# Kernel optimization log

Measured on AMD Instinct MI355X. Metric: run time of the kernel, lower is better.

The kernel has to match this reference:

```python
import jax, jax.numpy as jnp
import numpy as np

N = 50000      # atoms
E = 800000     # edges (avg degree 16)
F = 32         # feature channels
NB = 8         # Bessel basis size
RCUT = 20.0    # Angstrom cutoff (covers the 1nm box)
EV2KJ = 96.4853
NM2A = 10.0


def setup_inputs() -> dict:
    key = jax.random.key(0)
    ks = jax.random.split(key, 12)
    return {
        "positions": jax.random.uniform(ks[0], (N, 3), jnp.float32),      # nm
        "masses": jax.random.uniform(ks[1], (N,), jnp.float32),
        "type_embed": jax.random.normal(ks[2], (3, F), jnp.float32),
        "W_rad1": jax.random.normal(ks[3], (NB, F), jnp.float32) * 0.3,
        "b_rad1": jax.random.normal(ks[4], (F,), jnp.float32) * 0.1,
        "W_rad2": jax.random.normal(ks[5], (F, 2 * F), jnp.float32) * 0.3,
        "W_self": jax.random.normal(ks[6], (F, F), jnp.float32) * 0.3,
        "W_out1": jax.random.normal(ks[7], (2 * F, F), jnp.float32) * 0.3,
        "b_out1": jax.random.normal(ks[8], (F,), jnp.float32) * 0.1,
        "W_out2": jax.random.normal(ks[9], (F, 1), jnp.float32) * 0.3,
        "atom_types": jax.random.randint(ks[10], (N,), 0, 3),
        "edge_index": jax.random.randint(ks[11], (2, E), 0, N),
    }


def reference(positions, masses, type_embed, W_rad1, b_rad1, W_rad2,
              W_self, W_out1, b_out1, W_out2, atom_types, edge_index):
    src, dst = edge_index[0], edge_index[1]

    def energy_eV(pos_A):
        rel = pos_A[dst] - pos_A[src]                       # [E,3] gather
        r = jnp.sqrt(jnp.sum(rel * rel, axis=-1) + 1e-12)   # [E]
        rhat = rel / r[:, None]
        # Bessel radial basis with p=6 polynomial cutoff envelope
        x = r / RCUT
        n = jnp.arange(1, NB + 1, dtype=pos_A.dtype)
        basis = jnp.sin(jnp.pi * n[None, :] * x[:, None]) / r[:, None]  # [E,NB]
        p = 6.0
        env = (1.0 - (p + 1) * (p + 2) / 2 * x**p
               + p * (p + 2) * x**(p + 1)
               - p * (p + 1) / 2 * x**(p + 2))
        env = jnp.where(x < 1.0, env, 0.0)
        rw = jax.nn.silu(basis @ W_rad1 + b_rad1) @ W_rad2   # [E,2F]
        rw = rw * env[:, None]
        w0, w1 = rw[:, :F], rw[:, F:]
        h = type_embed[atom_types]                           # [N,F]
        hs = h[src]                                          # [E,F] gather
        m0 = hs * w0                                         # l=0 messages
        m1 = (hs * w1)[:, :, None] * rhat[:, None, :]        # l=1 messages [E,F,3]
        s = jax.ops.segment_sum(m0, dst, num_segments=N)     # scatter-add
        v = jax.ops.segment_sum(m1.reshape(E, F * 3), dst, num_segments=N)
        v = v.reshape(N, F, 3)
        vnorm = jnp.sqrt(jnp.sum(v * v, axis=-1) + 1e-12)    # invariant [N,F]
        feats = jnp.concatenate([h + s @ W_self, vnorm], axis=1)  # [N,2F]
        per_atom = jax.nn.silu(feats @ W_out1 + b_out1) @ W_out2  # [N,1]
        return jnp.sum(per_atom)

    pos_A = positions * NM2A
    e_eV, g = jax.value_and_grad(energy_eV)(pos_A)
    energy = e_eV * EV2KJ                                    # kJ/mol
    forces = -g * (EV2KJ * NM2A)                             # kJ/mol/nm
    # COM drift correction: mass-weighted net-force subtraction
    net = jnp.sum(forces, axis=0, keepdims=True)
    forces = forces - (masses[:, None] / jnp.sum(masses)) * net
    return energy, forces
```

## Files before the change

### kernel.cpp

```cpp
#include <hip/hip_runtime.h>
#include <math.h>

#define FDIM 32
#define NBASIS 8
#define QP 40
#define DS 18
#define BINW 4096
#define DCAP 4096
#define GSPLIT 8

constexpr float RCUT_C = 20.0f;
constexpr float PI_F = 3.14159265358979323846f;
constexpr float EV2KJ_C = 96.4853f;
constexpr float NM2A_C = 10.0f;

typedef _Float16 f16x8 __attribute__((ext_vector_type(8)));
typedef _Float16 f16x4 __attribute__((ext_vector_type(4)));
typedef float f32x4 __attribute__((ext_vector_type(4)));

__device__ __forceinline__ float sigmoidf_(float z) { return 1.0f / (1.0f + __expf(-z)); }

__device__ __forceinline__ unsigned int pk2_(float a, float b) {
    unsigned short lo = __builtin_bit_cast(unsigned short, (_Float16)a);
    unsigned short hi = __builtin_bit_cast(unsigned short, (_Float16)b);
    return (unsigned int)lo | ((unsigned int)hi << 16);
}
__device__ __forceinline__ float lo16_(unsigned int v) {
    return (float)__builtin_bit_cast(_Float16, (unsigned short)(v & 0xffffu));
}
__device__ __forceinline__ float hi16_(unsigned int v) {
    return (float)__builtin_bit_cast(_Float16, (unsigned short)(v >> 16));
}

__global__ __launch_bounds__(256) void hist_buckets(
    const int* __restrict__ eidx, int* __restrict__ dbcnt, int* __restrict__ sbcnt,
    int E, int dsh, int ssh, int nbd, int nbs)
{
    __shared__ int ld[512];
    __shared__ int ls[64];
    for (int i = threadIdx.x; i < nbd; i += 256) ld[i] = 0;
    for (int i = threadIdx.x; i < nbs; i += 256) ls[i] = 0;
    __syncthreads();
    for (int e = blockIdx.x * 256 + threadIdx.x; e < E; e += gridDim.x * 256) {
        int s = eidx[e];
        int d = eidx[E + e];
        atomicAdd(&ld[d >> dsh], 1);
        atomicAdd(&ls[s >> ssh], 1);
    }
    __syncthreads();
    for (int i = threadIdx.x; i < nbd; i += 256) if (ld[i]) atomicAdd(&dbcnt[i], ld[i]);
    for (int i = threadIdx.x; i < nbs; i += 256) if (ls[i]) atomicAdd(&sbcnt[i], ls[i]);
}

__global__ __launch_bounds__(512) void scan_bases(
    const int* __restrict__ dbcnt, const int* __restrict__ sbcnt,
    int* __restrict__ dbbase, int* __restrict__ sbbase, int nbd, int nbs)
{
    __shared__ int buf[512];
    const int t = threadIdx.x;
    int v = (t < nbd) ? dbcnt[t] : 0;
    buf[t] = v;
    __syncthreads();
    for (int off = 1; off < 512; off <<= 1) {
        int u = (t >= off) ? buf[t - off] : 0;
        __syncthreads();
        buf[t] += u;
        __syncthreads();
    }
    if (t < nbd) dbbase[t] = buf[t] - v;
    if (t == 511) dbbase[nbd] = buf[511];
    __syncthreads();
    int v2 = (t < nbs) ? sbcnt[t] : 0;
    buf[t] = v2;
    __syncthreads();
    for (int off = 1; off < 512; off <<= 1) {
        int u = (t >= off) ? buf[t - off] : 0;
        __syncthreads();
        buf[t] += u;
        __syncthreads();
    }
    if (t < nbs) sbbase[t] = buf[t] - v2;
    if (t == 511) sbbase[nbs] = buf[511];
}

__global__ __launch_bounds__(256) void bin_dst(
    const int* __restrict__ eidx, const int* __restrict__ dbbase,
    int* __restrict__ dbcur, int2* __restrict__ order_sd,
    int E, int dsh, int nbd)
{
    __shared__ int2 rec[BINW];
    __shared__ int lcnt[512], lbase[512], lofs[512];
    const int t = threadIdx.x;
    const int w0 = blockIdx.x * BINW;
    const int n = min(BINW, E - w0);
    if (n <= 0) return;
    for (int i = t; i < nbd; i += 256) lcnt[i] = 0;
    __syncthreads();
    for (int i = t; i < n; i += 256) {
        int e = w0 + i;
        int2 r = make_int2(eidx[e], eidx[E + e]);
        rec[i] = r;
        atomicAdd(&lcnt[r.y >> dsh], 1);
    }
    __syncthreads();
    for (int i = t; i < nbd; i += 256) {
        int c = lcnt[i];
        lbase[i] = c ? atomicAdd(&dbcur[i], c) : 0;
        lofs[i] = 0;
    }
    __syncthreads();
    for (int i = t; i < n; i += 256) {
        int2 r = rec[i];
        int b = r.y >> dsh;
        int pos = lbase[b] + atomicAdd(&lofs[b], 1);
        order_sd[dbbase[b] + pos] = r;
    }
}

__global__ __launch_bounds__(256) void sort_bucket(
    int2* __restrict__ order_sd, const int* __restrict__ dbbase,
    int* __restrict__ sbcur, const int* __restrict__ sbbase,
    int2* __restrict__ srcbin, int dsh, int ssh)
{
    __shared__ int2 rec[DCAP];
    __shared__ int c128[128], o128[128];
    __shared__ int sc[64], sbres[64], so[64];
    const int b = blockIdx.x, t = threadIdx.x;
    const int base = dbbase[b];
    const int cnt = dbbase[b + 1] - base;
    const bool dosort = (dsh <= 7);
    const int kmask = (1 << dsh) - 1;

    for (int start = 0; start < cnt; start += DCAP) {
        const int n = min(DCAP, cnt - start);
        if (t < 128) c128[t] = 0;
        if (t < 64) sc[t] = 0;
        __syncthreads();
        for (int i = t; i < n; i += 256) {
            int2 r = order_sd[base + start + i];
            rec[i] = r;
            if (dosort) atomicAdd(&c128[r.y & kmask], 1);
            atomicAdd(&sc[r.x >> ssh], 1);
        }
        __syncthreads();
        int v0 = (t < 128) ? c128[t] : 0;
        __syncthreads();
        for (int off = 1; off < 128; off <<= 1) {
            int u = (t < 128 && t >= off) ? c128[t - off] : 0;
            __syncthreads();
            if (t < 128) c128[t] += u;
            __syncthreads();
        }
        if (t < 128) o128[t] = c128[t] - v0;
        if (t < 64) {
            int c = sc[t];
            sbres[t] = c ? atomicAdd(&sbcur[t], c) : 0;
            so[t] = 0;
        }
        __syncthreads();
        for (int i = t; i < n; i += 256) {
            int2 r = rec[i];
            int p;
            if (dosort) {
                int pos = atomicAdd(&o128[r.y & kmask], 1);
                p = base + start + pos;
                order_sd[p] = r;
            } else {
                p = base + start + i;
            }
            int sb2 = r.x >> ssh;
            int slot = sbres[sb2] + atomicAdd(&so[sb2], 1);
            srcbin[sbbase[sb2] + slot] = make_int2(r.x, p);
        }
        __syncthreads();
    }
}

__global__ __launch_bounds__(64) void pack_wfrag(
    const float* __restrict__ Wr1, const float* __restrict__ Wr2,
    _Float16* __restrict__ wpack)
{
    const int lane = threadIdx.x;
    const int kb = (lane >> 4) * 8, nb = lane & 15;
    _Float16* o = wpack + (size_t)lane * 64;
    #pragma unroll
    for (int t = 0; t < 2; t++)
        #pragma unroll
        for (int j = 0; j < 8; j++) {
            int k = kb + j;
            o[t * 8 + j] = (k < 8) ? (_Float16)Wr1[k * FDIM + t * 16 + nb] : (_Float16)0.0f;
        }
    #pragma unroll
    for (int t = 0; t < 4; t++)
        #pragma unroll
        for (int j = 0; j < 8; j++)
            o[16 + t * 8 + j] = (_Float16)Wr2[(kb + j) * 64 + t * 16 + nb];
    #pragma unroll
    for (int t = 0; t < 2; t++)
        #pragma unroll
        for (int j = 0; j < 8; j++) {
            int k = kb + j;
            o[48 + t * 8 + j] = (k >= 8 && k < 16) ? (_Float16)Wr1[(k - 8) * FDIM + t * 16 + nb]
                                                   : (_Float16)0.0f;
        }
}

__global__ __launch_bounds__(256) void edge_fwd_mfma(
    const float* __restrict__ pos, const int* __restrict__ types,
    const int2* __restrict__ order_sd,
    const _Float16* __restrict__ wpack, const float* __restrict__ br1,
    const float* __restrict__ temb,
    float* __restrict__ s_acc, float* __restrict__ v_acc, int E)
{
    __shared__ __align__(16) _Float16 sR[4][2560];
    __shared__ float sSt[4][32][4];
    __shared__ int sTy[4][32];
    __shared__ int sKey[4][32];
    __shared__ float sTemb[96];

    const int lane = threadIdx.x & 63;
    const int l32 = threadIdx.x & 31;
    const int hw = (threadIdx.x >> 5) & 1;
    const int w = threadIdx.x >> 6;
    const int gbase = blockIdx.x * 128 + w * 32;

    for (int i = threadIdx.x; i < 96; i += 256) sTemb[i] = temb[i];
    __syncthreads();

    const int kb = (lane >> 4) * 8;
    const f16x8* wp = (const f16x8*)(wpack + (size_t)lane * 64);
    f16x8 bz[2] = { wp[0], wp[1] };
    f16x8 bf[4] = { wp[2], wp[3], wp[4], wp[5] };

    if (lane < 32) {
        const int ed = l32;
        const int p = gbase + ed;
        const bool vld = (p < E);
        int2 sd = vld ? order_sd[p] : make_int2(0, 0);
        float rx = (pos[sd.y * 3 + 0] - pos[sd.x * 3 + 0]) * NM2A_C;
        float ry = (pos[sd.y * 3 + 1] - pos[sd.x * 3 + 1]) * NM2A_C;
        float rz = (pos[sd.y * 3 + 2] - pos[sd.x * 3 + 2]) * NM2A_C;
        float r2 = rx * rx + ry * ry + rz * rz + 1e-12f;
        float r = sqrtf(r2);
        float rinv = 1.0f / r;
        float x = r * (1.0f / RCUT_C);
        float x2 = x * x, x4 = x2 * x2, x6 = x4 * x2, x7 = x6 * x, x8 = x6 * x2;
        float env = (x < 1.0f) ? (1.0f - 28.0f * x6 + 48.0f * x7 - 21.0f * x8) : 0.0f;

        float th = PI_F * x, s1, c1;
        __sincosf(th, &s1, &c1);
        float sp = 0.0f, sn = s1;
        _Float16 av[8];
        #pragma unroll
        for (int n = 0; n < NBASIS; n++) {
            av[n] = (_Float16)(sn * rinv);
            float snx = 2.0f * c1 * sn - sp; sp = sn; sn = snx;
        }
        _Float16* dstA = &sR[w][(ed < 16 ? 0 : 640) + (ed & 15) * QP];
        *(f16x8*)&dstA[0] = *(f16x8*)&av[0];
        *(float4*)&dstA[8]  = make_float4(0.f, 0.f, 0.f, 0.f);
        *(float4*)&dstA[16] = make_float4(0.f, 0.f, 0.f, 0.f);
        *(float4*)&dstA[24] = make_float4(0.f, 0.f, 0.f, 0.f);
        sSt[w][ed][0] = env;
        sSt[w][ed][1] = rx * rinv;
        sSt[w][ed][2] = ry * rinv;
        sSt[w][ed][3] = rz * rinv;
        sTy[w][ed] = types[sd.x];
        sKey[w][ed] = vld ? sd.y : -1;
    }

    {
        const int me = lane & 15;
        f16x8 a1a = *(const f16x8*)&sR[w][me * QP + kb];
        f16x8 a1b = *(const f16x8*)&sR[w][640 + me * QP + kb];
        const f32x4 z4 = {0.f, 0.f, 0.f, 0.f};
        f32x4 Dz0a = __builtin_amdgcn_mfma_f32_16x16x32_f16(a1a, bz[0], z4, 0, 0, 0);
        f32x4 Dz1a = __builtin_amdgcn_mfma_f32_16x16x32_f16(a1a, bz[1], z4, 0, 0, 0);
        f32x4 Dz0b = __builtin_amdgcn_mfma_f32_16x16x32_f16(a1b, bz[0], z4, 0, 0, 0);
        f32x4 Dz1b = __builtin_amdgcn_mfma_f32_16x16x32_f16(a1b, bz[1], z4, 0, 0, 0);
        const int f0 = lane & 15, e0 = (lane >> 4) * 4;
        const float bb0 = br1[f0], bb1 = br1[16 + f0];
        #pragma unroll
        for (int t = 0; t < 2; t++) {
            f32x4 Dza = t ? Dz1a : Dz0a;
            f32x4 Dzb = t ? Dz1b : Dz0b;
            float bb = t ? bb1 : bb0;
            #pragma unroll
            for (int r = 0; r < 4; r++) {
                float za = Dza[r] + bb;
                float zb = Dzb[r] + bb;
                sR[w][1280 + (e0 + r) * QP + t * 16 + f0] = (_Float16)(za * sigmoidf_(za));
                sR[w][1920 + (e0 + r) * QP + t * 16 + f0] = (_Float16)(zb * sigmoidf_(zb));
            }
        }
    }

    {
        const int me = lane & 15;
        f16x8 aqa = *(const f16x8*)&sR[w][1280 + me * QP + kb];
        f16x8 aqb = *(const f16x8*)&sR[w][1920 + me * QP + kb];
        const int cb = lane & 15, e0 = (lane >> 4) * 4;
        float hev[2][2][4];
        #pragma unroll
        for (int tl = 0; tl < 2; tl++)
            #pragma unroll
            for (int fp = 0; fp < 2; fp++)
                #pragma unroll
                for (int r = 0; r < 4; r++) {
                    int ed = tl * 16 + e0 + r;
                    hev[tl][fp][r] = sTemb[sTy[w][ed] * 32 + fp * 16 + cb] * sSt[w][ed][0];
                }
        const f32x4 z4 = {0.f, 0.f, 0.f, 0.f};
        unsigned int* DU = (unsigned int*)&sR[w][0];
        #pragma unroll
        for (int fp = 0; fp < 2; fp++) {
            f32x4 a0 = __builtin_amdgcn_mfma_f32_16x16x32_f16(aqa, bf[fp],     z4, 0, 0, 0);
            f32x4 a1 = __builtin_amdgcn_mfma_f32_16x16x32_f16(aqa, bf[fp + 2], z4, 0, 0, 0);
            f32x4 b0 = __builtin_amdgcn_mfma_f32_16x16x32_f16(aqb, bf[fp],     z4, 0, 0, 0);
            f32x4 b1 = __builtin_amdgcn_mfma_f32_16x16x32_f16(aqb, bf[fp + 2], z4, 0, 0, 0);
            #pragma unroll
            for (int r = 0; r < 4; r++) {
                float ha = hev[0][fp][r], hb = hev[1][fp][r];
                DU[(e0 + r) * 32 + fp * 16 + cb]        = pk2_(a0[r] * ha, a1[r] * ha);
                DU[(16 + e0 + r) * 32 + fp * 16 + cb]   = pk2_(b0[r] * hb, b1[r] * hb);
            }
        }
    }

    const unsigned int* DU = (const unsigned int*)&sR[w][0];
    int runKey = -1;
    float sAcc = 0.f, vXA = 0.f, vYA = 0.f, vZA = 0.f;
    #pragma unroll
    for (int t = 0; t < 2; t++) {
        #pragma unroll
        for (int i = 0; i < 8; i++) {
            const int m = t * 16 + hw * 8 + i;
            const int p = gbase + m;
            if (p >= E) break;
            int k = sKey[w][m];
            if (k != runKey) {
                if (runKey >= 0) {
                    unsafeAtomicAdd(&s_acc[(size_t)runKey * 32 + l32], sAcc);
                    unsafeAtomicAdd(&v_acc[(size_t)runKey * 96 + 0 * 32 + l32], vXA);
                    unsafeAtomicAdd(&v_acc[(size_t)runKey * 96 + 1 * 32 + l32], vYA);
                    unsafeAtomicAdd(&v_acc[(size_t)runKey * 96 + 2 * 32 + l32], vZA);
                }
                runKey = k;
                sAcc = vXA = vYA = vZA = 0.f;
            }
            unsigned int qp = DU[m * 32 + l32];
            float s0 = lo16_(qp);
            float h1 = hi16_(qp);
            sAcc += s0;
            vXA += h1 * sSt[w][m][1];
            vYA += h1 * sSt[w][m][2];
            vZA += h1 * sSt[w][m][3];
        }
    }
    if (runKey >= 0) {
        unsafeAtomicAdd(&s_acc[(size_t)runKey * 32 + l32], sAcc);
        unsafeAtomicAdd(&v_acc[(size_t)runKey * 96 + 0 * 32 + l32], vXA);
        unsafeAtomicAdd(&v_acc[(size_t)runKey * 96 + 1 * 32 + l32], vYA);
        unsafeAtomicAdd(&v_acc[(size_t)runKey * 96 + 2 * 32 + l32], vZA);
    }
}

__global__ __launch_bounds__(256) void atom_mlp(
    const int* __restrict__ types, const float* __restrict__ temb,
    const float* __restrict__ Wself, const float* __restrict__ Wo1,
    const float* __restrict__ bo1, const float* __restrict__ Wo2,
    const float* __restrict__ s_acc, const float* __restrict__ v_acc,
    float* __restrict__ g_all, float* __restrict__ out, int N)
{
    __shared__ float sWs[FDIM * FDIM], sWsT[FDIM * FDIM];
    __shared__ float sWo1[2 * FDIM * FDIM], sWo1T[2 * FDIM * FDIM];
    __shared__ float sb[FDIM], sW2o[FDIM], sTE[96];
    __shared__ float gred[8];
    for (int i = threadIdx.x; i < FDIM * FDIM; i += 256) {
        sWs[i] = Wself[i];
        sWsT[i] = Wself[(i & 31) * FDIM + (i >> 5)];
    }
    for (int i = threadIdx.x; i < 2 * FDIM * FDIM; i += 256) {
        sWo1[i] = Wo1[i];
        sWo1T[i] = Wo1[(i & 63) * FDIM + (i >> 6)];
    }
    for (int i = threadIdx.x; i < FDIM; i += 256) { sb[i] = bo1[i]; sW2o[i] = Wo2[i]; }
    for (int i = threadIdx.x; i < 96; i += 256) sTE[i] = temb[i];
    __syncthreads();

    const int lane = threadIdx.x & 31;
    const int g = threadIdx.x >> 5;
    float eAcc = 0.0f;

    for (int it = 0; it < 8; it++) {
        int a = blockIdx.x * 64 + it * 8 + g;
        const bool valid = (a < N);
        if (!valid) a = 0;

        float sv = s_acc[(size_t)a * FDIM + lane];
        float vx = v_acc[(size_t)a * 96 + 0 * 32 + lane];
        float vy = v_acc[(size_t)a * 96 + 1 * 32 + lane];
        float vz = v_acc[(size_t)a * 96 + 2 * 32 + lane];
        float h = sTE[types[a] * FDIM + lane];
        float vn = sqrtf(vx * vx + vy * vy + vz * vz + 1e-12f);

        float row = h;
        #pragma unroll
        for (int f = 0; f < FDIM; f++) {
            float t = __shfl(sv, f, 32);
            row += t * sWs[f * FDIM + lane];
        }
        float u = sb[lane];
        #pragma unroll
        for (int j = 0; j < FDIM; j++) {
            float rv = __shfl(row, j, 32);
            float vv = __shfl(vn, j, 32);
            u += rv * sWo1[j * FDIM + lane] + vv * sWo1[(j + FDIM) * FDIM + lane];
        }
        float sg = sigmoidf_(u);
        float au = u * sg;
        float pa = valid ? au * sW2o[lane] : 0.0f;
        #pragma unroll
        for (int m = 16; m; m >>= 1) pa += __shfl_xor(pa, m, 32);
        if (lane == 0) eAcc += pa;

        float gu = sW2o[lane] * (sg * (1.0f + u * (1.0f - sg)));
        float gfr = 0.0f, gfv = 0.0f;
        #pragma unroll
        for (int k = 0; k < FDIM; k++) {
            float gv_ = __shfl(gu, k, 32);
            gfr += gv_ * sWo1T[k * 64 + lane];
            gfv += gv_ * sWo1T[k * 64 + 32 + lane];
        }
        float gs = 0.0f;
        #pragma unroll
        for (int k = 0; k < FDIM; k++) {
            float gr = __shfl(gfr, k, 32);
            gs += gr * sWsT[k * FDIM + lane];
        }
        if (valid) {
            float sc = gfv / vn;
            *(float4*)&g_all[(size_t)a * 128 + lane * 4] =
                make_float4(gs, sc * vx, sc * vy, sc * vz);
        }
    }
    if (lane == 0) gred[g] = eAcc;
    __syncthreads();
    if (threadIdx.x == 0) {
        float t = 0.0f;
        #pragma unroll
        for (int i = 0; i < 8; i++) t += gred[i];
        unsafeAtomicAdd(out, t * EV2KJ_C);
    }
}

__global__ __launch_bounds__(256) void edge_bwd_mfma(
    const float* __restrict__ pos, const int* __restrict__ types,
    const int2* __restrict__ order_sd,
    const _Float16* __restrict__ wpack, const float* __restrict__ br1,
    const float* __restrict__ temb,
    const float* __restrict__ g_all,
    float* __restrict__ forces, float4* __restrict__ fbuf, int E)
{
    __shared__ __align__(16) _Float16 sR1[4][1280];
    __shared__ __align__(16) _Float16 sR2[4][1152];
    __shared__ int   sTy[4][16];
    __shared__ float sTemb[96];

    const int lane = threadIdx.x & 63;
    const int l16 = lane & 15;
    const int w = threadIdx.x >> 6;
    const int gbase = blockIdx.x * 64 + w * 16;

    for (int i = threadIdx.x; i < 96; i += 256) sTemb[i] = temb[i];
    __syncthreads();

    const int kb = (lane >> 4) * 8;
    const f16x8* wp = (const f16x8*)(wpack + (size_t)lane * 64);
    f16x8 bz[2] = { wp[0], wp[1] };
    f16x8 bf[4] = { wp[2], wp[3], wp[4], wp[5] };
    f16x8 bt[2] = { wp[6], wp[7] };

    const int p_e = gbase + l16;
    const bool valid = (p_e < E);
    int2 sd = valid ? order_sd[p_e] : make_int2(0, 0);
    const int srcI = sd.x, dstI = sd.y;
    const int key = valid ? sd.y : (-2 - l16);
    (void)srcI;

    float rinv = 1.f, env = 0.f, denv = 0.f, rhx = 0.f, rhy = 0.f, rhz = 0.f;
    if (lane < 16) {
        float rx = (pos[sd.y * 3 + 0] - pos[sd.x * 3 + 0]) * NM2A_C;
        float ry = (pos[sd.y * 3 + 1] - pos[sd.x * 3 + 1]) * NM2A_C;
        float rz = (pos[sd.y * 3 + 2] - pos[sd.x * 3 + 2]) * NM2A_C;
        float r2 = rx * rx + ry * ry + rz * rz + 1e-12f;
        float r = sqrtf(r2);
        rinv = 1.0f / r;
        float x = r * (1.0f / RCUT_C);
        float x2 = x * x, x4 = x2 * x2, x5 = x4 * x, x6 = x4 * x2, x7 = x6 * x, x8 = x6 * x2;
        env = (x < 1.0f) ? (1.0f - 28.0f * x6 + 48.0f * x7 - 21.0f * x8) : 0.0f;
        denv = (x < 1.0f) ? (-168.0f * x5 + 336.0f * x6 - 168.0f * x7) * (1.0f / RCUT_C) : 0.0f;
        rhx = rx * rinv; rhy = ry * rinv; rhz = rz * rinv;

        float th = PI_F * x, s1, c1;
        __sincosf(th, &s1, &c1);
        float sp = 0.0f, sn = s1, cp = 1.0f, cn = c1;
        _Float16 av[16];
        #pragma unroll
        for (int n = 0; n < NBASIS; n++) {
            float basis = sn * rinv;
            float dbdr = (PI_F * (float)(n + 1) * (1.0f / RCUT_C)) * cn * rinv - basis * rinv;
            av[n] = (_Float16)basis;
            av[8 + n] = (_Float16)dbdr;
            float snx = 2.0f * c1 * sn - sp; sp = sn; sn = snx;
            float cnx = 2.0f * c1 * cn - cp; cp = cn; cn = cnx;
        }
        _Float16* dstA = &sR1[w][l16 * QP];
        *(f16x8*)&dstA[0] = *(f16x8*)&av[0];
        *(f16x8*)&dstA[8] = *(f16x8*)&av[8];
        *(float4*)&dstA[16] = make_float4(0.f, 0.f, 0.f, 0.f);
        *(float4*)&dstA[24] = make_float4(0.f, 0.f, 0.f, 0.f);
        sTy[w][l16] = types[sd.x];
    }

    {
        const int me = lane & 15;
        f16x8 a1 = *(const f16x8*)&sR1[w][me * QP + kb];
        const f32x4 z4 = {0.f, 0.f, 0.f, 0.f};
        f32x4 Dz0 = __builtin_amdgcn_mfma_f32_16x16x32_f16(a1, bz[0], z4, 0, 0, 0);
        f32x4 Dz1 = __builtin_amdgcn_mfma_f32_16x16x32_f16(a1, bz[1], z4, 0, 0, 0);
        f32x4 Dt0 = __builtin_amdgcn_mfma_f32_16x16x32_f16(a1, bt[0], z4, 0, 0, 0);
        f32x4 Dt1 = __builtin_amdgcn_mfma_f32_16x16x32_f16(a1, bt[1], z4, 0, 0, 0);
        const int f0 = lane & 15, e0 = (lane >> 4) * 4;
        const float bb0 = br1[f0], bb1 = br1[16 + f0];
        #pragma unroll
        for (int t = 0; t < 2; t++) {
            f32x4 Dz = t ? Dz1 : Dz0;
            f32x4 Dt = t ? Dt1 : Dt0;
            float bb = t ? bb1 : bb0;
            #pragma unroll
            for (int r = 0; r < 4; r++) {
                float z = Dz[r] + bb;
                float sg = sigmoidf_(z);
                sR2[w][(e0 + r) * QP + t * 16 + f0] = (_Float16)(z * sg);
                sR1[w][640 + (e0 + r) * QP + t * 16 + f0] =
                    (_Float16)((sg * (1.0f + z * (1.0f - sg))) * Dt[r]);
            }
        }
    }

    {
        const int me = lane & 15;
        f16x8 aq = *(const f16x8*)&sR2[w][me * QP + kb];
        f16x8 at = *(const f16x8*)&sR1[w][640 + me * QP + kb];
        const int cb = lane & 15, e0 = (lane >> 4) * 4;
        float hsv[2][4];
        #pragma unroll
        for (int r = 0; r < 4; r++) {
            int ty = sTy[w][e0 + r];
            hsv[0][r] = sTemb[ty * 32 + cb];
            hsv[1][r] = sTemb[ty * 32 + 16 + cb];
        }
        const f32x4 z4 = {0.f, 0.f, 0.f, 0.f};
        unsigned int* DqU = (unsigned int*)&sR1[w][0];
        unsigned int* DtU = (unsigned int*)&sR2[w][0];
        #pragma unroll
        for (int fp = 0; fp < 2; fp++) {
            f32x4 q0 = __builtin_amdgcn_mfma_f32_16x16x32_f16(aq, bf[fp],     z4, 0, 0, 0);
            f32x4 q1 = __builtin_amdgcn_mfma_f32_16x16x32_f16(aq, bf[fp + 2], z4, 0, 0, 0);
            f32x4 t0 = __builtin_amdgcn_mfma_f32_16x16x32_f16(at, bf[fp],     z4, 0, 0, 0);
            f32x4 t1 = __builtin_amdgcn_mfma_f32_16x16x32_f16(at, bf[fp + 2], z4, 0, 0, 0);
            unsigned int pq[4], pt[4];
            #pragma unroll
            for (int r = 0; r < 4; r++) {
                float h = hsv[fp][r];
                pq[r] = pk2_(q0[r] * h, q1[r] * h);
                pt[r] = pk2_(t0[r] * h, t1[r] * h);
            }
            const int f = fp * 16 + cb;
            *(uint2*)&DqU[f * DS + e0]     = make_uint2(pq[0], pq[1]);
            *(uint2*)&DqU[f * DS + e0 + 2] = make_uint2(pq[2], pq[3]);
            *(uint2*)&DtU[f * DS + e0]     = make_uint2(pt[0], pt[1]);
            *(uint2*)&DtU[f * DS + e0 + 2] = make_uint2(pt[2], pt[3]);
        }
    }

    {
        const unsigned int* DqU = (const unsigned int*)&sR1[w][0];
        const unsigned int* DtU = (const unsigned int*)&sR2[w][0];
        const int fb = (lane >> 4) * 8;
        const float* gb = g_all + (size_t)dstI * 128;
        float Aa = 0.f, Bb = 0.f, Cc = 0.f, Pp = 0.f;
        float Ap = 0.f, Bp = 0.f, Cp = 0.f, Qq = 0.f;
        #pragma unroll
        for (int ff = 0; ff < 8; ff++) {
            const int f = fb + ff;
            unsigned int qp = DqU[f * DS + l16];
            unsigned int tp = DtU[f * DS + l16];
            float rw0 = lo16_(qp), rw1 = hi16_(qp);
            float u0 = lo16_(tp), u1 = hi16_(tp);
            float4 g4 = *(const float4*)(gb + f * 4);
            Pp += rw0 * g4.x; Qq += u0 * g4.x;
            Aa += rw1 * g4.y; Bb += rw1 * g4.z; Cc += rw1 * g4.w;
            Ap += u1 * g4.y;  Bp += u1 * g4.z;  Cp += u1 * g4.w;
        }
        Pp += __shfl_xor(Pp, 16, 64); Qq += __shfl_xor(Qq, 16, 64);
        Aa += __shfl_xor(Aa, 16, 64); Bb += __shfl_xor(Bb, 16, 64);
        Cc += __shfl_xor(Cc, 16, 64); Ap += __shfl_xor(Ap, 16, 64);
        Bp += __shfl_xor(Bp, 16, 64); Cp += __shfl_xor(Cp, 16, 64);
        Pp += __shfl_xor(Pp, 32, 64); Qq += __shfl_xor(Qq, 32, 64);
        Aa += __shfl_xor(Aa, 32, 64); Bb += __shfl_xor(Bb, 32, 64);
        Cc += __shfl_xor(Cc, 32, 64); Ap += __shfl_xor(Ap, 32, 64);
        Bp += __shfl_xor(Bp, 32, 64); Cp += __shfl_xor(Cp, 32, 64);

        if (lane < 16) {
            float Gx = env * Aa, Gy = env * Bb, Gz = env * Cc;
            float genv = Pp + rhx * Aa + rhy * Bb + rhz * Cc;
            float pc = env * (Qq + rhx * Ap + rhy * Bp + rhz * Cp) + genv * denv;
            float dotg = Gx * rhx + Gy * rhy + Gz * rhz;
            float cx = pc * rhx + (Gx - dotg * rhx) * rinv;
            float cy = pc * rhy + (Gy - dotg * rhy) * rinv;
            float cz = pc * rhz + (Gz - dotg * rhz) * rinv;

            const float SC = EV2KJ_C * NM2A_C;
            if (valid) fbuf[p_e] = make_float4(SC * cx, SC * cy, SC * cz, 0.0f);

            int kk = key;
            #pragma unroll
            for (int d = 1; d < 16; d <<= 1) {
                float ux = __shfl_up(cx, d, 32);
                float uy = __shfl_up(cy, d, 32);
                float uz = __shfl_up(cz, d, 32);
                int uk = __shfl_up(kk, d, 32);
                if (l16 >= d && uk == kk) { cx += ux; cy += uy; cz += uz; }
            }
            int nk = __shfl_down(kk, 1, 32);
            bool leader = (l16 == 15) || (nk != kk);
            if (valid && leader) {
                unsafeAtomicAdd(&forces[(size_t)dstI * 3 + 0], -SC * cx);
                unsafeAtomicAdd(&forces[(size_t)dstI * 3 + 1], -SC * cy);
                unsafeAtomicAdd(&forces[(size_t)dstI * 3 + 2], -SC * cz);
            }
        }
    }
}

__global__ __launch_bounds__(256) void gather_src(
    float* __restrict__ forces, const int* __restrict__ sbbase,
    const int2* __restrict__ srcbin, const float4* __restrict__ fbuf,
    int ssh, int N)
{
    __shared__ float acc[3072];
    const int wg = blockIdx.x;
    const int b = wg / GSPLIT, part = wg % GSPLIT;
    const int base = sbbase[b];
    const int cnt = sbbase[b + 1] - base;
    const int r0 = base + (int)((long long)cnt * part / GSPLIT);
    const int r1 = base + (int)((long long)cnt * (part + 1) / GSPLIT);
    const int abase = b << ssh;
    const bool lok = (ssh <= 10);
    for (int i = threadIdx.x; i < 3072; i += 256) acc[i] = 0.f;
    __syncthreads();
    for (int i = r0 + threadIdx.x; i < r1; i += 256) {
        int2 r = srcbin[i];
        float4 f = fbuf[r.y];
        if (lok) {
            int la = r.x - abase;
            atomicAdd(&acc[la * 3 + 0], f.x);
            atomicAdd(&acc[la * 3 + 1], f.y);
            atomicAdd(&acc[la * 3 + 2], f.z);
        } else {
            unsafeAtomicAdd(&forces[(size_t)r.x * 3 + 0], f.x);
            unsafeAtomicAdd(&forces[(size_t)r.x * 3 + 1], f.y);
            unsafeAtomicAdd(&forces[(size_t)r.x * 3 + 2], f.z);
        }
    }
    __syncthreads();
    if (lok) {
        for (int la = threadIdx.x; la < 1024; la += 256) {
            int a = abase + la;
            if (a < N) {
                float ax = acc[la * 3 + 0], ay = acc[la * 3 + 1], az = acc[la * 3 + 2];
                if (ax != 0.f || ay != 0.f || az != 0.f) {
                    unsafeAtomicAdd(&forces[(size_t)a * 3 + 0], ax);
                    unsafeAtomicAdd(&forces[(size_t)a * 3 + 1], ay);
                    unsafeAtomicAdd(&forces[(size_t)a * 3 + 2], az);
                }
            }
        }
    }
}

__global__ __launch_bounds__(256) void reduce_net(
    const float* __restrict__ f, const float* __restrict__ masses,
    float* __restrict__ accum, int N)
{
    float nx = 0, ny = 0, nz = 0, ms = 0;
    for (int i = blockIdx.x * 256 + threadIdx.x; i < N; i += gridDim.x * 256) {
        nx += f[i * 3 + 0]; ny += f[i * 3 + 1]; nz += f[i * 3 + 2]; ms += masses[i];
    }
    #pragma unroll
    for (int m = 32; m; m >>= 1) {
        nx += __shfl_xor(nx, m, 64);
        ny += __shfl_xor(ny, m, 64);
        nz += __shfl_xor(nz, m, 64);
        ms += __shfl_xor(ms, m, 64);
    }
    __shared__ float red[4][4];
    int w = threadIdx.x >> 6;
    if ((threadIdx.x & 63) == 0) { red[w][0] = nx; red[w][1] = ny; red[w][2] = nz; red[w][3] = ms; }
    __syncthreads();
    if (threadIdx.x == 0) {
        float a0 = 0, a1 = 0, a2 = 0, a3 = 0;
        for (int i = 0; i < 4; i++) { a0 += red[i][0]; a1 += red[i][1]; a2 += red[i][2]; a3 += red[i][3]; }
        unsafeAtomicAdd(accum + 0, a0);
        unsafeAtomicAdd(accum + 1, a1);
        unsafeAtomicAdd(accum + 2, a2);
        unsafeAtomicAdd(accum + 3, a3);
    }
}

__global__ __launch_bounds__(256) void correct_forces(
    float* __restrict__ f, const float* __restrict__ masses,
    const float* __restrict__ accum, int N)
{
    int i = blockIdx.x * 256 + threadIdx.x;
    if (i < N) {
        float c = masses[i] / accum[3];
        f[i * 3 + 0] -= c * accum[0];
        f[i * 3 + 1] -= c * accum[1];
        f[i * 3 + 2] -= c * accum[2];
    }
}

extern "C" void kernel_launch(void* const* d_in, const int* in_sizes, int n_in,
                              void* d_out, int out_size, void* d_ws, size_t ws_size,
                              hipStream_t stream)
{
    (void)n_in; (void)ws_size;
    const float* pos    = (const float*)d_in[0];
    const float* masses = (const float*)d_in[1];
    const float* temb   = (const float*)d_in[2];
    const float* Wr1    = (const float*)d_in[3];
    const float* br1    = (const float*)d_in[4];
    const float* Wr2    = (const float*)d_in[5];
    const float* Wself  = (const float*)d_in[6];
    const float* Wo1    = (const float*)d_in[7];
    const float* bo1    = (const float*)d_in[8];
    const float* Wo2    = (const float*)d_in[9];
    const int* types    = (const int*)d_in[10];
    const int* eidx     = (const int*)d_in[11];
    const int N = in_sizes[1];
    const int E = in_sizes[11] / 2;

    float* out = (float*)d_out;
    float* forces = out + 1;

    int dsh = 7;  while (((N + (1 << dsh) - 1) >> dsh) > 512) dsh++;
    int nbd = (N + (1 << dsh) - 1) >> dsh;
    int ssh = 10; while (((N + (1 << ssh) - 1) >> ssh) > 64) ssh++;
    int nbs = (N + (1 << ssh) - 1) >> ssh;

    float* ws = (float*)d_ws;
    float* s_acc = ws;
    float* v_acc = s_acc + (size_t)N * FDIM;
    float* g_all = v_acc + (size_t)N * 96;
    float* accum = g_all + (size_t)N * 128;
    int* meta = (int*)(accum + 4);
    int* dbcnt  = meta;
    int* sbcnt  = dbcnt + 512;
    int* dbcur  = sbcnt + 64;
    int* sbcur  = dbcur + 512;
    int* dbbase = sbcur + 64;
    int* sbbase = dbbase + 513;
    int2* order_sd = (int2*)(((uintptr_t)(sbbase + 65) + 15) & ~(uintptr_t)15);
    int2* srcbin   = order_sd + E;
    float4* fbuf   = (float4*)(((uintptr_t)(srcbin + E) + 15) & ~(uintptr_t)15);
    _Float16* wpack = (_Float16*)(fbuf + E);

    hipMemsetAsync(d_out, 0, (size_t)out_size * sizeof(float), stream);
    hipMemsetAsync(s_acc, 0, (size_t)N * 128 * sizeof(float), stream);
    hipMemsetAsync(meta, 0, 1152 * sizeof(int), stream);
    hipMemsetAsync(accum, 0, 4 * sizeof(float), stream);

    hist_buckets<<<512, 256, 0, stream>>>(eidx, dbcnt, sbcnt, E, dsh, ssh, nbd, nbs);
    scan_bases<<<1, 512, 0, stream>>>(dbcnt, sbcnt, dbbase, sbbase, nbd, nbs);
    int nBin = (E + BINW - 1) / BINW;
    bin_dst<<<nBin, 256, 0, stream>>>(eidx, dbbase, dbcur, order_sd, E, dsh, nbd);
    sort_bucket<<<nbd, 256, 0, stream>>>(order_sd, dbbase, sbcur, sbbase, srcbin, dsh, ssh);
    pack_wfrag<<<1, 64, 0, stream>>>(Wr1, Wr2, wpack);

    int nAtomBlocks = (N + 63) / 64;
    int nFwdBlocks = (E + 127) / 128;
    int nBwdBlocks = (E + 63) / 64;
    edge_fwd_mfma<<<nFwdBlocks, 256, 0, stream>>>(pos, types, order_sd,
                                                  wpack, br1, temb,
                                                  s_acc, v_acc, E);
    atom_mlp<<<nAtomBlocks, 256, 0, stream>>>(types, temb, Wself, Wo1, bo1, Wo2,
                                              s_acc, v_acc, g_all, out, N);
    edge_bwd_mfma<<<nBwdBlocks, 256, 0, stream>>>(pos, types, order_sd,
                                                  wpack, br1, temb,
                                                  g_all, forces, fbuf, E);
    gather_src<<<nbs * GSPLIT, 256, 0, stream>>>(forces, sbbase, srcbin, fbuf, ssh, N);
    reduce_net<<<64, 256, 0, stream>>>(forces, masses, accum, N);
    correct_forces<<<(N + 255) / 256, 256, 0, stream>>>(forces, masses, accum, N);
}
```

Baseline: 454.8 us.

## Map one atom per thread in atom MLP instead of one atom per half-wave

Rewrites the per-atom MLP kernel so each thread processes a whole atom with 32-element register arrays and broadcast float4 LDS weight reads, in place of 32 lanes per atom with shuffles. Blocks shrink to 64 threads, and the transposed weight copies are no longer needed. The intent is to drop the shuffle traffic and per-lane redundancy. The cost is very high register pressure (several 32-float arrays live at once), possible spilling, lower occupancy, and strided, uncoalesced per-thread global loads and stores across atoms.

```diff
diff --git a/kernel.cpp b/kernel.cpp
--- a/kernel.cpp
+++ b/kernel.cpp
@@ -365,92 +365,136 @@
     }
 }
 
-__global__ __launch_bounds__(256) void atom_mlp(
+__global__ __launch_bounds__(64) void atom_mlp(
     const int* __restrict__ types, const float* __restrict__ temb,
     const float* __restrict__ Wself, const float* __restrict__ Wo1,
     const float* __restrict__ bo1, const float* __restrict__ Wo2,
     const float* __restrict__ s_acc, const float* __restrict__ v_acc,
     float* __restrict__ g_all, float* __restrict__ out, int N)
 {
-    __shared__ float sWs[FDIM * FDIM], sWsT[FDIM * FDIM];
-    __shared__ float sWo1[2 * FDIM * FDIM], sWo1T[2 * FDIM * FDIM];
-    __shared__ float sb[FDIM], sW2o[FDIM], sTE[96];
-    __shared__ float gred[8];
-    for (int i = threadIdx.x; i < FDIM * FDIM; i += 256) {
-        sWs[i] = Wself[i];
-        sWsT[i] = Wself[(i & 31) * FDIM + (i >> 5)];
-    }
-    for (int i = threadIdx.x; i < 2 * FDIM * FDIM; i += 256) {
-        sWo1[i] = Wo1[i];
-        sWo1T[i] = Wo1[(i & 63) * FDIM + (i >> 6)];
-    }
-    for (int i = threadIdx.x; i < FDIM; i += 256) { sb[i] = bo1[i]; sW2o[i] = Wo2[i]; }
-    for (int i = threadIdx.x; i < 96; i += 256) sTE[i] = temb[i];
-    __syncthreads();
-
-    const int lane = threadIdx.x & 31;
-    const int g = threadIdx.x >> 5;
-    float eAcc = 0.0f;
-
-    for (int it = 0; it < 8; it++) {
-        int a = blockIdx.x * 64 + it * 8 + g;
-        const bool valid = (a < N);
-        if (!valid) a = 0;
-
-        float sv = s_acc[(size_t)a * FDIM + lane];
-        float vx = v_acc[(size_t)a * 96 + 0 * 32 + lane];
-        float vy = v_acc[(size_t)a * 96 + 1 * 32 + lane];
-        float vz = v_acc[(size_t)a * 96 + 2 * 32 + lane];
-        float h = sTE[types[a] * FDIM + lane];
-        float vn = sqrtf(vx * vx + vy * vy + vz * vz + 1e-12f);
-
-        float row = h;
-        #pragma unroll
-        for (int f = 0; f < FDIM; f++) {
-            float t = __shfl(sv, f, 32);
-            row += t * sWs[f * FDIM + lane];
-        }
-        float u = sb[lane];
-        #pragma unroll
-        for (int j = 0; j < FDIM; j++) {
-            float rv = __shfl(row, j, 32);
-            float vv = __shfl(vn, j, 32);
-            u += rv * sWo1[j * FDIM + lane] + vv * sWo1[(j + FDIM) * FDIM + lane];
-        }
-        float sg = sigmoidf_(u);
-        float au = u * sg;
-        float pa = valid ? au * sW2o[lane] : 0.0f;
-        #pragma unroll
-        for (int m = 16; m; m >>= 1) pa += __shfl_xor(pa, m, 32);
-        if (lane == 0) eAcc += pa;
-
-        float gu = sW2o[lane] * (sg * (1.0f + u * (1.0f - sg)));
-        float gfr = 0.0f, gfv = 0.0f;
-        #pragma unroll
-        for (int k = 0; k < FDIM; k++) {
-            float gv_ = __shfl(gu, k, 32);
-            gfr += gv_ * sWo1T[k * 64 + lane];
-            gfv += gv_ * sWo1T[k * 64 + 32 + lane];
-        }
-        float gs = 0.0f;
-        #pragma unroll
-        for (int k = 0; k < FDIM; k++) {
-            float gr = __shfl(gfr, k, 32);
-            gs += gr * sWsT[k * FDIM + lane];
-        }
-        if (valid) {
-            float sc = gfv / vn;
-            *(float4*)&g_all[(size_t)a * 128 + lane * 4] =
-                make_float4(gs, sc * vx, sc * vy, sc * vz);
-        }
-    }
-    if (lane == 0) gred[g] = eAcc;
-    __syncthreads();
-    if (threadIdx.x == 0) {
-        float t = 0.0f;
-        #pragma unroll
-        for (int i = 0; i < 8; i++) t += gred[i];
-        unsafeAtomicAdd(out, t * EV2KJ_C);
+    __shared__ __align__(16) float sWs[FDIM * FDIM];
+    __shared__ __align__(16) float sWo1[2 * FDIM * FDIM];
+    __shared__ __align__(16) float sb[FDIM], sW2o[FDIM], sTE[96];
+    const int t = threadIdx.x;
+    for (int i = t; i < FDIM * FDIM; i += 64) sWs[i] = Wself[i];
+    for (int i = t; i < 2 * FDIM * FDIM; i += 64) sWo1[i] = Wo1[i];
+    if (t < FDIM) { sb[t] = bo1[t]; sW2o[t] = Wo2[t]; }
+    for (int i = t; i < 96; i += 64) sTE[i] = temb[i];
+    __syncthreads();
+
+    int a = blockIdx.x * 64 + t;
+    const bool valid = (a < N);
+    if (!valid) a = 0;
+
+    float s[32];
+    #pragma unroll
+    for (int q = 0; q < 8; q++) {
+        float4 v = *(const float4*)&s_acc[(size_t)a * FDIM + q * 4];
+        s[q * 4 + 0] = v.x; s[q * 4 + 1] = v.y; s[q * 4 + 2] = v.z; s[q * 4 + 3] = v.w;
+    }
+    const int ty = types[a];
+    float row[32];
+    #pragma unroll
+    for (int j = 0; j < 32; j++) row[j] = sTE[ty * FDIM + j];
+    #pragma unroll
+    for (int k = 0; k < 32; k++) {
+        float sk = s[k];
+        #pragma unroll
+        for (int q = 0; q < 8; q++) {
+            float4 wv = *(const float4*)&sWs[k * 32 + q * 4];
+            row[q * 4 + 0] += sk * wv.x; row[q * 4 + 1] += sk * wv.y;
+            row[q * 4 + 2] += sk * wv.z; row[q * 4 + 3] += sk * wv.w;
+        }
+    }
+
+    float vn[32];
+    #pragma unroll
+    for (int q = 0; q < 8; q++) {
+        float4 x4 = *(const float4*)&v_acc[(size_t)a * 96 +      q * 4];
+        float4 y4 = *(const float4*)&v_acc[(size_t)a * 96 + 32 + q * 4];
+        float4 z4 = *(const float4*)&v_acc[(size_t)a * 96 + 64 + q * 4];
+        vn[q * 4 + 0] = sqrtf(x4.x * x4.x + y4.x * y4.x + z4.x * z4.x + 1e-12f);
+        vn[q * 4 + 1] = sqrtf(x4.y * x4.y + y4.y * y4.y + z4.y * z4.y + 1e-12f);
+        vn[q * 4 + 2] = sqrtf(x4.z * x4.z + y4.z * y4.z + z4.z * z4.z + 1e-12f);
+        vn[q * 4 + 3] = sqrtf(x4.w * x4.w + y4.w * y4.w + z4.w * z4.w + 1e-12f);
+    }
+
+    float u[32];
+    #pragma unroll
+    for (int j = 0; j < 32; j++) u[j] = sb[j];
+    #pragma unroll
+    for (int k = 0; k < 32; k++) {
+        float rk = row[k], vk = vn[k];
+        #pragma unroll
+        for (int q = 0; q < 8; q++) {
+            float4 w1 = *(const float4*)&sWo1[k * 32 + q * 4];
+            float4 w2 = *(const float4*)&sWo1[(k + 32) * 32 + q * 4];
+            u[q * 4 + 0] += rk * w1.x + vk * w2.x;
+            u[q * 4 + 1] += rk * w1.y + vk * w2.y;
+            u[q * 4 + 2] += rk * w1.z + vk * w2.z;
+            u[q * 4 + 3] += rk * w1.w + vk * w2.w;
+        }
+    }
+
+    float pa = 0.0f;
+    #pragma unroll
+    for (int j = 0; j < 32; j++) {
+        float z = u[j];
+        float sg = sigmoidf_(z);
+        pa += z * sg * sW2o[j];
+        u[j] = sW2o[j] * (sg * (1.0f + z * (1.0f - sg)));
+    }
+    if (!valid) pa = 0.0f;
+    #pragma unroll
+    for (int m = 32; m; m >>= 1) pa += __shfl_xor(pa, m, 64);
+    if (t == 0) unsafeAtomicAdd(out, pa * EV2KJ_C);
+
+    float gfr[32], gfv[32];
+    #pragma unroll
+    for (int j = 0; j < 32; j++) {
+        float ar = 0.f, av = 0.f;
+        #pragma unroll
+        for (int q = 0; q < 8; q++) {
+            float4 w1 = *(const float4*)&sWo1[j * 32 + q * 4];
+            float4 w2 = *(const float4*)&sWo1[(j + 32) * 32 + q * 4];
+            ar += u[q * 4 + 0] * w1.x + u[q * 4 + 1] * w1.y
+                + u[q * 4 + 2] * w1.z + u[q * 4 + 3] * w1.w;
+            av += u[q * 4 + 0] * w2.x + u[q * 4 + 1] * w2.y
+                + u[q * 4 + 2] * w2.z + u[q * 4 + 3] * w2.w;
+        }
+        gfr[j] = ar; gfv[j] = av;
+    }
+
+    float gs[32];
+    #pragma unroll
+    for (int j = 0; j < 32; j++) {
+        float acc = 0.f;
+        #pragma unroll
+        for (int q = 0; q < 8; q++) {
+            float4 wv = *(const float4*)&sWs[j * 32 + q * 4];
+            acc += gfr[q * 4 + 0] * wv.x + gfr[q * 4 + 1] * wv.y
+                 + gfr[q * 4 + 2] * wv.z + gfr[q * 4 + 3] * wv.w;
+        }
+        gs[j] = acc;
+    }
+
+    if (valid) {
+        #pragma unroll
+        for (int q = 0; q < 8; q++) {
+            float4 x4 = *(const float4*)&v_acc[(size_t)a * 96 +      q * 4];
+            float4 y4 = *(const float4*)&v_acc[(size_t)a * 96 + 32 + q * 4];
+            float4 z4 = *(const float4*)&v_acc[(size_t)a * 96 + 64 + q * 4];
+            #pragma unroll
+            for (int c = 0; c < 4; c++) {
+                int j = q * 4 + c;
+                float vx = (c == 0) ? x4.x : (c == 1) ? x4.y : (c == 2) ? x4.z : x4.w;
+                float vy = (c == 0) ? y4.x : (c == 1) ? y4.y : (c == 2) ? y4.z : y4.w;
+                float vz = (c == 0) ? z4.x : (c == 1) ? z4.y : (c == 2) ? z4.z : z4.w;
+                float sc = gfv[j] / vn[j];
+                *(float4*)&g_all[(size_t)a * 128 + j * 4] =
+                    make_float4(gs[j], sc * vx, sc * vy, sc * vz);
+            }
+        }
     }
 }
 
@@ -796,8 +840,8 @@
     edge_fwd_mfma<<<nFwdBlocks, 256, 0, stream>>>(pos, types, order_sd,
                                                   wpack, br1, temb,
                                                   s_acc, v_acc, E);
-    atom_mlp<<<nAtomBlocks, 256, 0, stream>>>(types, temb, Wself, Wo1, bo1, Wo2,
-                                              s_acc, v_acc, g_all, out, N);
+    atom_mlp<<<nAtomBlocks, 64, 0, stream>>>(types, temb, Wself, Wo1, bo1, Wo2,
+                                             s_acc, v_acc, g_all, out, N);
     edge_bwd_mfma<<<nBwdBlocks, 256, 0, stream>>>(pos, types, order_sd,
                                                   wpack, br1, temb,
                                                   g_all, forces, fbuf, E);
```

New measurement: 486.2 us. +6.9%, slower.
